# Optimization experiments

Hardware: AMD Instinct MI355X
Metric: run time of the kernel (lower is better)

## Reference

```python
import jax, jax.numpy as jnp
import numpy as np

EMBED_DIM = 128
HEADS = 4
HEAD_DIM = EMBED_DIM // HEADS
HIDDEN = EMBED_DIM * 4


def setup_inputs() -> dict:
    key = jax.random.key(0)
    ks = jax.random.split(key, 12)
    s = 0.02
    return {
        "x": jax.random.normal(ks[0], (4, 4096, EMBED_DIM), dtype=jnp.float32),
        "ln1_g": jnp.ones((EMBED_DIM,), jnp.float32),
        "ln1_b": jnp.zeros((EMBED_DIM,), jnp.float32),
        "qkv_w": jax.random.normal(ks[1], (EMBED_DIM, 3 * EMBED_DIM), jnp.float32) * s,
        "qkv_b": jnp.zeros((3 * EMBED_DIM,), jnp.float32),
        "proj_w": jax.random.normal(ks[2], (EMBED_DIM, EMBED_DIM), jnp.float32) * s,
        "proj_b": jnp.zeros((EMBED_DIM,), jnp.float32),
        "ln2_g": jnp.ones((EMBED_DIM,), jnp.float32),
        "ln2_b": jnp.zeros((EMBED_DIM,), jnp.float32),
        "mlp_w1": jax.random.normal(ks[3], (EMBED_DIM, HIDDEN), jnp.float32) * s,
        "mlp_b1": jnp.zeros((HIDDEN,), jnp.float32),
        "mlp_w2": jax.random.normal(ks[4], (HIDDEN, EMBED_DIM), jnp.float32) * s,
        "mlp_b2": jnp.zeros((EMBED_DIM,), jnp.float32),
    }


def _layernorm(x, g, b, eps=1e-5):
    mu = jnp.mean(x, axis=-1, keepdims=True)
    var = jnp.var(x, axis=-1, keepdims=True)
    return (x - mu) * jax.lax.rsqrt(var + eps) * g + b


def _msa(x, qkv_w, qkv_b, proj_w, proj_b):
    B, N, C = x.shape
    qkv = x @ qkv_w + qkv_b                       # [B,N,3C]
    qkv = qkv.reshape(B, N, 3, HEADS, HEAD_DIM)
    q, k, v = jnp.moveaxis(qkv, 2, 0)             # each [B,N,H,D]
    # scores: [B,H,N,N]
    attn = jnp.einsum("bnhd,bmhd->bhnm", q, k) / jnp.sqrt(jnp.float32(HEAD_DIM))
    attn = jax.nn.softmax(attn, axis=-1)
    out = jnp.einsum("bhnm,bmhd->bnhd", attn, v).reshape(B, N, C)
    return out @ proj_w + proj_b


def reference(x, ln1_g, ln1_b, qkv_w, qkv_b, proj_w, proj_b,
              ln2_g, ln2_b, mlp_w1, mlp_b1, mlp_w2, mlp_b2):
    # dropout is identity in eval mode
    x = x + _msa(_layernorm(x, ln1_g, ln1_b), qkv_w, qkv_b, proj_w, proj_b)
    h = _layernorm(x, ln2_g, ln2_b)
    h = jax.nn.gelu(h @ mlp_w1 + mlp_b1, approximate=False)
    x = x + (h @ mlp_w2 + mlp_b2)
    return x
```

## Files before the change

kernel.cpp:

```cpp
#include <hip/hip_runtime.h>
#include <hip/hip_bf16.h>
#include <math.h>

#define NSEQ   4096
#define CDIM   128
#define HD     32

typedef __attribute__((ext_vector_type(8))) short short8;
typedef __attribute__((ext_vector_type(4))) short short4v;
typedef __attribute__((ext_vector_type(4))) float f32x4;

#define QSCL (0.17677669529663687f * 1.4426950408889634f)

__device__ inline unsigned short f2bf(float f){
  union { float f; unsigned u; } v; v.f = f;
  return (unsigned short)((v.u + 0x7fffu + ((v.u >> 16) & 1u)) >> 16);
}
__device__ inline float bf2f(unsigned short u){
  union { unsigned u; float f; } v; v.u = ((unsigned)u) << 16;
  return v.f;
}
__device__ inline void gload_lds16(const unsigned short* g, unsigned short* l){
  __builtin_amdgcn_global_load_lds(
      (const __attribute__((address_space(1))) void*)g,
      (__attribute__((address_space(3))) void*)l, 16, 0, 0);
}


__global__ __launch_bounds__(256) void k_pack(
    const float* __restrict__ qkv_w, const float* __restrict__ qkv_b,
    const float* __restrict__ proj_w, const float* __restrict__ mlp_w1,
    const float* __restrict__ mlp_w2, unsigned short* __restrict__ wpack,
    float* __restrict__ bqs)
{
  const int gt = blockIdx.x * 256 + threadIdx.x;
  const int tile = gt >> 6, lane = gt & 63;
  const float* src; int N, KT, toff, dstoff; float scale = 1.f;
  if (tile < 96)       { src = qkv_w;  N = 384; KT = 4;  toff = tile;       dstoff = 0; }
  else if (tile < 128) { src = proj_w; N = 128; KT = 4;  toff = tile - 96;  dstoff = 49152; }
  else if (tile < 256) { src = mlp_w1; N = 512; KT = 4;  toff = tile - 128; dstoff = 65536; }
  else                 { src = mlp_w2; N = 128; KT = 16; toff = tile - 256; dstoff = 131072; }
  const int ct = toff / KT, kt = toff % KT;
  if (tile < 96 && ct < 8) scale = QSCL;
  const int row0 = kt * 32 + (lane >> 4) * 8, col = ct * 16 + (lane & 15);
  short8 v;
  #pragma unroll
  for (int i = 0; i < 8; i++)
    v[i] = (short)f2bf(src[(size_t)(row0 + i) * N + col] * scale);
  *(short8*)(wpack + dstoff + ((size_t)(ct * KT + kt) * 64 + lane) * 8) = v;
  if (gt < 384) bqs[gt] = qkv_b[gt] * (gt < 128 ? QSCL : 1.f);
}

__global__ __launch_bounds__(512) void k_qkv(
    const float* __restrict__ x, const float* __restrict__ g,
    const float* __restrict__ b, const unsigned short* __restrict__ wpack,
    const float* __restrict__ bqs, unsigned short* __restrict__ qkv)
{
  __shared__ unsigned short xn[64 * 128];
  const int tid = threadIdx.x;
  const int tok0 = blockIdx.x * 64;
  {
    const int grp = tid >> 5, l = tid & 31;
    #pragma unroll
    for (int it = 0; it < 4; it++){
      const int t = it * 16 + grp;
      const float4 xv = *(const float4*)(x + (size_t)(tok0 + t) * 128 + l * 4);
      float s  = xv.x + xv.y + xv.z + xv.w;
      float s2 = xv.x*xv.x + xv.y*xv.y + xv.z*xv.z + xv.w*xv.w;
      #pragma unroll
      for (int m = 1; m <= 16; m <<= 1){ s += __shfl_xor(s, m); s2 += __shfl_xor(s2, m); }
      const float mu = s * (1.f/128.f);
      const float rs = rsqrtf(s2 * (1.f/128.f) - mu*mu + 1e-5f);
      const int e = l * 4;
      const float4 gv = *(const float4*)(g + e), bv = *(const float4*)(b + e);
      short4v pk;
      pk[0] = (short)f2bf((xv.x - mu)*rs*gv.x + bv.x);
      pk[1] = (short)f2bf((xv.y - mu)*rs*gv.y + bv.y);
      pk[2] = (short)f2bf((xv.z - mu)*rs*gv.z + bv.z);
      pk[3] = (short)f2bf((xv.w - mu)*rs*gv.w + bv.w);
      const int bl = l >> 1;
      const int slot = bl * 64 + (t & 48) + ((t & 15) ^ bl);
      *(short4v*)(xn + slot * 8 + (l & 1) * 4) = pk;
    }
  }
  __syncthreads();
  const int wv = tid >> 6, lane = tid & 63, r = lane & 15, cg = lane >> 4;
  const int rt = wv & 3, ct0 = (wv >> 2) * 12;
  short8 af[4];
  #pragma unroll
  for (int kt = 0; kt < 4; kt++){
    const int bl = kt * 4 + cg;
    const int slot = bl * 64 + rt * 16 + (r ^ bl);
    af[kt] = *(const short8*)(xn + slot * 8);
  }
  const int bidx = tok0 >> 12, nloc = (tok0 & (NSEQ - 1)) + rt * 16 + cg * 4;
  for (int ct = ct0; ct < ct0 + 12; ct++){
    f32x4 acc = {0.f, 0.f, 0.f, 0.f};
    const unsigned short* bp = wpack + ((size_t)(ct * 4) * 64 + lane) * 8;
    #pragma unroll
    for (int kt = 0; kt < 4; kt++)
      acc = __builtin_amdgcn_mfma_f32_16x16x32_bf16(af[kt], *(const short8*)(bp + kt * 512), acc, 0, 0, 0);
    const int col = ct * 16 + r;
    const float bi = bqs[col];
    if (ct < 8){
      const int cc = col & 127, h = cc >> 5, d = cc & 31;
      unsigned short* plane = qkv + ((size_t)bidx * 4 + h) * (NSEQ * HD);
      #pragma unroll
      for (int reg = 0; reg < 4; reg++)
        plane[(size_t)(nloc + reg) * HD + d] = f2bf(acc[reg] + bi);
    } else if (ct < 16){
      const int cc = col & 127, h = cc >> 5, d = cc & 31;
      unsigned short* plane = qkv + ((size_t)16 + bidx * 4 + h) * (NSEQ * HD);
      const int t16 = ((tok0 & (NSEQ - 1)) >> 4) + rt;
      #pragma unroll
      for (int reg = 0; reg < 4; reg++)
        plane[(size_t)t16 * 512 + (d >> 3) * 128 + (cg * 4 + reg) * 8 + (d & 7)]
            = f2bf(acc[reg] + bi);
    } else {
      const int vct = ct - 16, h = vct >> 1, half = vct & 1;
      unsigned short* plane = qkv + ((size_t)32 + bidx * 4 + h) * (NSEQ * HD);
      const size_t ntile = (size_t)((tok0 & (NSEQ - 1)) >> 5) + (rt >> 1);
      const size_t vo = (ntile * 2 + half) * 512 + lane * 8 + (rt & 1) * 4;
      short4v pk;
      #pragma unroll
      for (int reg = 0; reg < 4; reg++) pk[reg] = (short)f2bf(acc[reg] + bi);
      *(short4v*)(plane + vo) = pk;
    }
  }
}

__global__ __launch_bounds__(512) void k_attn(
    const unsigned short* __restrict__ qkv, unsigned short* __restrict__ attnA)
{
  __shared__ unsigned short sbuf[16384];
  const int tid = threadIdx.x;
  const int lane = tid & 63, wv = tid >> 6;
  const int id = blockIdx.x;
  const int xcd = id & 7, seq = id >> 3;
  const int bh = xcd * 2 + (seq >> 4);
  const int qbase = (seq & 15) * 256 + wv * 32;
  const unsigned short* Q  = qkv + (size_t)bh * (NSEQ * HD);
  const unsigned short* Kc = qkv + (size_t)(16 + bh) * (NSEQ * HD);
  const unsigned short* Vc = qkv + (size_t)(32 + bh) * (NSEQ * HD);
  const int r = lane & 15, cg = lane >> 4;
  const short8 qf0 = *(const short8*)(Q + (size_t)(qbase + r) * HD + cg * 8);
  const short8 qf1 = *(const short8*)(Q + (size_t)(qbase + 16 + r) * HD + cg * 8);
  const unsigned short* gsrc = (wv < 4 ? Kc + wv * 512 : Vc + (wv - 4) * 512) + lane * 8;
  const int dst = wv * 512;
  union { unsigned u[4]; short8 s; } onesu;
  onesu.u[0] = 0x3F803F80u; onesu.u[1] = 0x3F803F80u;
  onesu.u[2] = 0x3F803F80u; onesu.u[3] = 0x3F803F80u;
  const short8 vones = onesu.s;
  f32x4 o00 = {0.f,0.f,0.f,0.f}, o01 = {0.f,0.f,0.f,0.f};
  f32x4 o10 = {0.f,0.f,0.f,0.f}, o11 = {0.f,0.f,0.f,0.f};
  f32x4 lacc0 = {0.f,0.f,0.f,0.f}, lacc1 = {0.f,0.f,0.f,0.f};
  const f32x4 zero = {0.f,0.f,0.f,0.f};
  gload_lds16(gsrc,        sbuf + 0 * 4096 + dst);
  gload_lds16(gsrc + 2048, sbuf + 1 * 4096 + dst);
  gload_lds16(gsrc + 4096, sbuf + 2 * 4096 + dst);
  for (int t = 0; t < 64; t++){
    asm volatile("s_waitcnt vmcnt(2) lgkmcnt(0)" ::: "memory");
    __builtin_amdgcn_sched_barrier(0);
    __builtin_amdgcn_s_barrier();
    __builtin_amdgcn_sched_barrier(0);
    const int tn = (t + 3 > 63) ? 63 : t + 3;
    gload_lds16(gsrc + (size_t)tn * 2048, sbuf + ((t + 3) & 3) * 4096 + dst);
    const unsigned short* skb = sbuf + (t & 3) * 4096;
    const unsigned short* svb = skb + 2048;
    #pragma unroll
    for (int ktp = 0; ktp < 2; ktp++){
      const short8 kaa = *(const short8*)(skb + (ktp * 2 + 0) * 512 + lane * 8);
      const short8 kab = *(const short8*)(skb + (ktp * 2 + 1) * 512 + lane * 8);
      const short8 va0 = *(const short8*)(svb + (ktp * 2 + 0) * 512 + lane * 8);
      const short8 va1 = *(const short8*)(svb + (ktp * 2 + 1) * 512 + lane * 8);
      const f32x4 s00 = __builtin_amdgcn_mfma_f32_16x16x32_bf16(kaa, qf0, zero, 0, 0, 0);
      const f32x4 s01 = __builtin_amdgcn_mfma_f32_16x16x32_bf16(kab, qf0, zero, 0, 0, 0);
      const f32x4 s10 = __builtin_amdgcn_mfma_f32_16x16x32_bf16(kaa, qf1, zero, 0, 0, 0);
      const f32x4 s11 = __builtin_amdgcn_mfma_f32_16x16x32_bf16(kab, qf1, zero, 0, 0, 0);
      float p00[4], p01[4], p10[4], p11[4];
      #pragma unroll
      for (int i = 0; i < 4; i++){
        p00[i] = __builtin_amdgcn_exp2f(s00[i]);
        p01[i] = __builtin_amdgcn_exp2f(s01[i]);
        p10[i] = __builtin_amdgcn_exp2f(s10[i]);
        p11[i] = __builtin_amdgcn_exp2f(s11[i]);
      }
      unsigned c0, c1, c2, c3, c4, c5, c6, c7;
      asm("v_cvt_pk_bf16_f32 %0, %1, %2" : "=v"(c0) : "v"(p00[0]), "v"(p00[1]));
      asm("v_cvt_pk_bf16_f32 %0, %1, %2" : "=v"(c1) : "v"(p00[2]), "v"(p00[3]));
      asm("v_cvt_pk_bf16_f32 %0, %1, %2" : "=v"(c2) : "v"(p01[0]), "v"(p01[1]));
      asm("v_cvt_pk_bf16_f32 %0, %1, %2" : "=v"(c3) : "v"(p01[2]), "v"(p01[3]));
      asm("v_cvt_pk_bf16_f32 %0, %1, %2" : "=v"(c4) : "v"(p10[0]), "v"(p10[1]));
      asm("v_cvt_pk_bf16_f32 %0, %1, %2" : "=v"(c5) : "v"(p10[2]), "v"(p10[3]));
      asm("v_cvt_pk_bf16_f32 %0, %1, %2" : "=v"(c6) : "v"(p11[0]), "v"(p11[1]));
      asm("v_cvt_pk_bf16_f32 %0, %1, %2" : "=v"(c7) : "v"(p11[2]), "v"(p11[3]));
      union { unsigned u[4]; short8 s; } pa, pb;
      pa.u[0] = c0; pa.u[1] = c1; pa.u[2] = c2; pa.u[3] = c3;
      pb.u[0] = c4; pb.u[1] = c5; pb.u[2] = c6; pb.u[3] = c7;
      o00 = __builtin_amdgcn_mfma_f32_16x16x32_bf16(va0, pa.s, o00, 0, 0, 0);
      o01 = __builtin_amdgcn_mfma_f32_16x16x32_bf16(va1, pa.s, o01, 0, 0, 0);
      o10 = __builtin_amdgcn_mfma_f32_16x16x32_bf16(va0, pb.s, o10, 0, 0, 0);
      o11 = __builtin_amdgcn_mfma_f32_16x16x32_bf16(va1, pb.s, o11, 0, 0, 0);
      lacc0 = __builtin_amdgcn_mfma_f32_16x16x32_bf16(vones, pa.s, lacc0, 0, 0, 0);
      lacc1 = __builtin_amdgcn_mfma_f32_16x16x32_bf16(vones, pb.s, lacc1, 0, 0, 0);
    }
  }
  asm volatile("s_waitcnt vmcnt(0)" ::: "memory");
  const float inv0 = 1.f / lacc0[0], inv1 = 1.f / lacc1[0];
  const int b = bh >> 2, h = bh & 3;
  unsigned short* pa = attnA + ((((size_t)b * NSEQ + qbase) >> 4) * 2048);
  short4v w0, w1, w2, w3;
  #pragma unroll
  for (int j = 0; j < 4; j++){
    w0[j] = (short)f2bf(o00[j] * inv0);
    w1[j] = (short)f2bf(o01[j] * inv0);
    w2[j] = (short)f2bf(o10[j] * inv1);
    w3[j] = (short)f2bf(o11[j] * inv1);
  }
  *(short4v*)(pa + (h * 4 + 0) * 128 + r * 8 + cg * 4)        = w0;
  *(short4v*)(pa + (h * 4 + 2) * 128 + r * 8 + cg * 4)        = w1;
  *(short4v*)(pa + 2048 + (h * 4 + 0) * 128 + r * 8 + cg * 4) = w2;
  *(short4v*)(pa + 2048 + (h * 4 + 2) * 128 + r * 8 + cg * 4) = w3;
}

__global__ __launch_bounds__(512, 6) void k_fused(
    const unsigned short* __restrict__ attnA, const float* __restrict__ x,
    const unsigned short* __restrict__ wpack, const float* __restrict__ pb,
    const float* __restrict__ g2, const float* __restrict__ b2,
    const float* __restrict__ b1, const float* __restrict__ b2m,
    float* __restrict__ out)
{
  __shared__ unsigned short afh[2][2048];
  __shared__ unsigned short sbb[32 * 128];
  __shared__ unsigned short afr[2][8192];
  const int tid = threadIdx.x, tok0 = blockIdx.x * 32;
  const int wv = tid >> 6, lane = tid & 63, r = lane & 15, cg = lane >> 4;
  const int rt = wv & 1, cgp = wv >> 1;
  {
    short8 af[4];
    const unsigned short* pa = attnA + ((size_t)((tok0 >> 4) + rt)) * 2048;
    #pragma unroll
    for (int kt = 0; kt < 4; kt++)
      af[kt] = *(const short8*)(pa + (kt * 4 + cg) * 128 + r * 8);
    const unsigned short* wp = wpack + 49152;
    for (int ct = cgp * 2; ct < cgp * 2 + 2; ct++){
      f32x4 acc = {0.f, 0.f, 0.f, 0.f};
      const unsigned short* bp = wp + ((size_t)(ct * 4) * 64 + lane) * 8;
      #pragma unroll
      for (int kt = 0; kt < 4; kt++)
        acc = __builtin_amdgcn_mfma_f32_16x16x32_bf16(af[kt], *(const short8*)(bp + kt * 512), acc, 0, 0, 0);
      const int col = ct * 16 + r;
      const float bi = pb[col];
      #pragma unroll
      for (int reg = 0; reg < 4; reg++){
        const int tl = rt * 16 + cg * 4 + reg;
        sbb[tl * 128 + col] = f2bf(acc[reg] + bi + x[(size_t)(tok0 + tl) * 128 + col]);
      }
    }
  }
  __syncthreads();
  {
    const int grp = tid >> 5, l = tid & 31;
    #pragma unroll
    for (int it = 0; it < 2; it++){
      const int t = it * 16 + grp;
      const short4v xb = *(const short4v*)(sbb + t * 128 + l * 4);
      const float x0 = bf2f((unsigned short)xb[0]), x1 = bf2f((unsigned short)xb[1]);
      const float x2 = bf2f((unsigned short)xb[2]), x3 = bf2f((unsigned short)xb[3]);
      float s  = x0 + x1 + x2 + x3;
      float s2 = x0*x0 + x1*x1 + x2*x2 + x3*x3;
      #pragma unroll
      for (int m = 1; m <= 16; m <<= 1){ s += __shfl_xor(s, m); s2 += __shfl_xor(s2, m); }
      const float mu = s * (1.f/128.f);
      const float rs = rsqrtf(s2 * (1.f/128.f) - mu*mu + 1e-5f);
      const int e = l * 4;
      const float4 gv = *(const float4*)(g2 + e), bv = *(const float4*)(b2 + e);
      short4v pk;
      pk[0] = (short)f2bf((x0 - mu)*rs*gv.x + bv.x);
      pk[1] = (short)f2bf((x1 - mu)*rs*gv.y + bv.y);
      pk[2] = (short)f2bf((x2 - mu)*rs*gv.z + bv.z);
      pk[3] = (short)f2bf((x3 - mu)*rs*gv.w + bv.w);
      *(short4v*)(&afh[t >> 4][(e >> 3) * 128 + (t & 15) * 8 + (e & 7)]) = pk;
    }
  }
  __syncthreads();
  {
    short8 hf[4];
    #pragma unroll
    for (int kt = 0; kt < 4; kt++)
      hf[kt] = *(const short8*)(&afh[rt][(kt * 4 + cg) * 128 + r * 8]);
    const unsigned short* w1 = wpack + 65536;
    for (int ct = cgp * 8; ct < cgp * 8 + 8; ct++){
      f32x4 acc = {0.f, 0.f, 0.f, 0.f};
      const unsigned short* bp = w1 + ((size_t)(ct * 4) * 64 + lane) * 8;
      #pragma unroll
      for (int kt = 0; kt < 4; kt++)
        acc = __builtin_amdgcn_mfma_f32_16x16x32_bf16(hf[kt], *(const short8*)(bp + kt * 512), acc, 0, 0, 0);
      const int col = ct * 16 + r;
      const float bi = b1[col];
      #pragma unroll
      for (int reg = 0; reg < 4; reg++){
        const float v = acc[reg] + bi;
        const float u = v * (2.3022077f + 0.10294324f * v * v);
        const float ge = v * __builtin_amdgcn_rcpf(1.f + __builtin_amdgcn_exp2f(-u));
        afr[rt][(col >> 3) * 128 + (cg * 4 + reg) * 8 + (col & 7)] = f2bf(ge);
      }
    }
  }
  __syncthreads();
  {
    const unsigned short* w2 = wpack + 131072;
    f32x4 acc0 = {0.f,0.f,0.f,0.f}, acc1 = {0.f,0.f,0.f,0.f};
    for (int kt = 0; kt < 16; kt++){
      const short8 a3 = *(const short8*)(&afr[rt][(kt * 4 + cg) * 128 + r * 8]);
      const unsigned short* bp0 = w2 + ((size_t)((cgp * 2 + 0) * 16 + kt) * 64 + lane) * 8;
      const unsigned short* bp1 = w2 + ((size_t)((cgp * 2 + 1) * 16 + kt) * 64 + lane) * 8;
      acc0 = __builtin_amdgcn_mfma_f32_16x16x32_bf16(a3, *(const short8*)(bp0), acc0, 0, 0, 0);
      acc1 = __builtin_amdgcn_mfma_f32_16x16x32_bf16(a3, *(const short8*)(bp1), acc1, 0, 0, 0);
    }
    #pragma unroll
    for (int c = 0; c < 2; c++){
      const f32x4 acc = c ? acc1 : acc0;
      const int col = (cgp * 2 + c) * 16 + r;
      const float bi = b2m[col];
      #pragma unroll
      for (int reg = 0; reg < 4; reg++){
        const int tl = rt * 16 + cg * 4 + reg;
        out[(size_t)(tok0 + tl) * 128 + col] = acc[reg] + bi + bf2f(sbb[tl * 128 + col]);
      }
    }
  }
}

extern "C" void kernel_launch(void* const* d_in, const int* in_sizes, int n_in,
                              void* d_out, int out_size, void* d_ws, size_t ws_size,
                              hipStream_t stream)
{
  const float* x      = (const float*)d_in[0];
  const float* ln1_g  = (const float*)d_in[1];
  const float* ln1_b  = (const float*)d_in[2];
  const float* qkv_w  = (const float*)d_in[3];
  const float* qkv_b  = (const float*)d_in[4];
  const float* proj_w = (const float*)d_in[5];
  const float* proj_b = (const float*)d_in[6];
  const float* ln2_g  = (const float*)d_in[7];
  const float* ln2_b  = (const float*)d_in[8];
  const float* mlp_w1 = (const float*)d_in[9];
  const float* mlp_b1 = (const float*)d_in[10];
  const float* mlp_w2 = (const float*)d_in[11];
  const float* mlp_b2 = (const float*)d_in[12];

  char* ws = (char*)d_ws;
  unsigned short* wpack = (unsigned short*)(ws);
  float*          bqs   = (float*)(ws + 393216);
  unsigned short* qkv   = (unsigned short*)(ws + 524288);
  unsigned short* attnA = (unsigned short*)(ws + 13107200);
  float* out = (float*)d_out;

  hipLaunchKernelGGL(k_pack, dim3(96), dim3(256), 0, stream,
                     qkv_w, qkv_b, proj_w, mlp_w1, mlp_w2, wpack, bqs);
  hipLaunchKernelGGL(k_qkv, dim3(256), dim3(512), 0, stream,
                     x, ln1_g, ln1_b, wpack, bqs, qkv);
  hipLaunchKernelGGL(k_attn, dim3(256), dim3(512), 0, stream, qkv, attnA);
  hipLaunchKernelGGL(k_fused, dim3(512), dim3(512), 0, stream,
                     attnA, x, wpack, proj_b, ln2_g, ln2_b,
                     mlp_b1, mlp_b2, out);
}
```

Baseline: 81.05 us.

## Retile attention to one query tile per wave and double grid size

The attention kernel now gives each wave 16 queries instead of 32. The grid doubles to 512 blocks. Each pipeline stage loads 256 keys and values into a 64KB LDS ring, using half the loop iterations. The aim is more blocks and waves per CU to hide latency and fill the device, at the cost of half the K/V reuse per wave, double total LDS read traffic, and a larger shared-memory footprint that may limit residency.

```diff
diff --git a/kernel.cpp b/kernel.cpp
--- a/kernel.cpp
+++ b/kernel.cpp
@@ -132,95 +132,81 @@
 __global__ __launch_bounds__(512) void k_attn(
     const unsigned short* __restrict__ qkv, unsigned short* __restrict__ attnA)
 {
-  __shared__ unsigned short sbuf[16384];
+  __shared__ unsigned short sbuf[32768];
   const int tid = threadIdx.x;
   const int lane = tid & 63, wv = tid >> 6;
   const int id = blockIdx.x;
   const int xcd = id & 7, seq = id >> 3;
-  const int bh = xcd * 2 + (seq >> 4);
-  const int qbase = (seq & 15) * 256 + wv * 32;
+  const int bh = xcd * 2 + (seq >> 5);
+  const int qbase = (seq & 31) * 128 + wv * 16;
   const unsigned short* Q  = qkv + (size_t)bh * (NSEQ * HD);
   const unsigned short* Kc = qkv + (size_t)(16 + bh) * (NSEQ * HD);
   const unsigned short* Vc = qkv + (size_t)(32 + bh) * (NSEQ * HD);
   const int r = lane & 15, cg = lane >> 4;
   const short8 qf0 = *(const short8*)(Q + (size_t)(qbase + r) * HD + cg * 8);
-  const short8 qf1 = *(const short8*)(Q + (size_t)(qbase + 16 + r) * HD + cg * 8);
-  const unsigned short* gsrc = (wv < 4 ? Kc + wv * 512 : Vc + (wv - 4) * 512) + lane * 8;
-  const int dst = wv * 512;
+  const unsigned short* gK = Kc + lane * 8;
+  const unsigned short* gV = Vc + lane * 8;
+  const int dK = wv * 512, dV = 4096 + wv * 512;
   union { unsigned u[4]; short8 s; } onesu;
   onesu.u[0] = 0x3F803F80u; onesu.u[1] = 0x3F803F80u;
   onesu.u[2] = 0x3F803F80u; onesu.u[3] = 0x3F803F80u;
   const short8 vones = onesu.s;
   f32x4 o00 = {0.f,0.f,0.f,0.f}, o01 = {0.f,0.f,0.f,0.f};
-  f32x4 o10 = {0.f,0.f,0.f,0.f}, o11 = {0.f,0.f,0.f,0.f};
-  f32x4 lacc0 = {0.f,0.f,0.f,0.f}, lacc1 = {0.f,0.f,0.f,0.f};
+  f32x4 lacc = {0.f,0.f,0.f,0.f};
   const f32x4 zero = {0.f,0.f,0.f,0.f};
-  gload_lds16(gsrc,        sbuf + 0 * 4096 + dst);
-  gload_lds16(gsrc + 2048, sbuf + 1 * 4096 + dst);
-  gload_lds16(gsrc + 4096, sbuf + 2 * 4096 + dst);
-  for (int t = 0; t < 64; t++){
-    asm volatile("s_waitcnt vmcnt(2) lgkmcnt(0)" ::: "memory");
+  #pragma unroll
+  for (int s = 0; s < 3; s++){
+    gload_lds16(gK + (size_t)(8 * s + wv) * 512, sbuf + s * 8192 + dK);
+    gload_lds16(gV + (size_t)(8 * s + wv) * 512, sbuf + s * 8192 + dV);
+  }
+  for (int t = 0; t < 32; t++){
+    asm volatile("s_waitcnt vmcnt(4) lgkmcnt(0)" ::: "memory");
     __builtin_amdgcn_sched_barrier(0);
     __builtin_amdgcn_s_barrier();
     __builtin_amdgcn_sched_barrier(0);
-    const int tn = (t + 3 > 63) ? 63 : t + 3;
-    gload_lds16(gsrc + (size_t)tn * 2048, sbuf + ((t + 3) & 3) * 4096 + dst);
-    const unsigned short* skb = sbuf + (t & 3) * 4096;
-    const unsigned short* svb = skb + 2048;
-    #pragma unroll
-    for (int ktp = 0; ktp < 2; ktp++){
+    const int tn = (t + 3 > 31) ? 31 : t + 3;
+    gload_lds16(gK + (size_t)(8 * tn + wv) * 512, sbuf + ((t + 3) & 3) * 8192 + dK);
+    gload_lds16(gV + (size_t)(8 * tn + wv) * 512, sbuf + ((t + 3) & 3) * 8192 + dV);
+    const unsigned short* skb = sbuf + (t & 3) * 8192;
+    const unsigned short* svb = skb + 4096;
+    #pragma unroll
+    for (int ktp = 0; ktp < 4; ktp++){
       const short8 kaa = *(const short8*)(skb + (ktp * 2 + 0) * 512 + lane * 8);
       const short8 kab = *(const short8*)(skb + (ktp * 2 + 1) * 512 + lane * 8);
-      const short8 va0 = *(const short8*)(svb + (ktp * 2 + 0) * 512 + lane * 8);
-      const short8 va1 = *(const short8*)(svb + (ktp * 2 + 1) * 512 + lane * 8);
+      const short8 va0 = *(const short8*)(svb + ktp * 1024 + lane * 8);
+      const short8 va1 = *(const short8*)(svb + ktp * 1024 + 512 + lane * 8);
       const f32x4 s00 = __builtin_amdgcn_mfma_f32_16x16x32_bf16(kaa, qf0, zero, 0, 0, 0);
       const f32x4 s01 = __builtin_amdgcn_mfma_f32_16x16x32_bf16(kab, qf0, zero, 0, 0, 0);
-      const f32x4 s10 = __builtin_amdgcn_mfma_f32_16x16x32_bf16(kaa, qf1, zero, 0, 0, 0);
-      const f32x4 s11 = __builtin_amdgcn_mfma_f32_16x16x32_bf16(kab, qf1, zero, 0, 0, 0);
-      float p00[4], p01[4], p10[4], p11[4];
+      float p0[4], p1[4];
       #pragma unroll
       for (int i = 0; i < 4; i++){
-        p00[i] = __builtin_amdgcn_exp2f(s00[i]);
-        p01[i] = __builtin_amdgcn_exp2f(s01[i]);
-        p10[i] = __builtin_amdgcn_exp2f(s10[i]);
-        p11[i] = __builtin_amdgcn_exp2f(s11[i]);
+        p0[i] = __builtin_amdgcn_exp2f(s00[i]);
+        p1[i] = __builtin_amdgcn_exp2f(s01[i]);
       }
-      unsigned c0, c1, c2, c3, c4, c5, c6, c7;
-      asm("v_cvt_pk_bf16_f32 %0, %1, %2" : "=v"(c0) : "v"(p00[0]), "v"(p00[1]));
-      asm("v_cvt_pk_bf16_f32 %0, %1, %2" : "=v"(c1) : "v"(p00[2]), "v"(p00[3]));
-      asm("v_cvt_pk_bf16_f32 %0, %1, %2" : "=v"(c2) : "v"(p01[0]), "v"(p01[1]));
-      asm("v_cvt_pk_bf16_f32 %0, %1, %2" : "=v"(c3) : "v"(p01[2]), "v"(p01[3]));
-      asm("v_cvt_pk_bf16_f32 %0, %1, %2" : "=v"(c4) : "v"(p10[0]), "v"(p10[1]));
-      asm("v_cvt_pk_bf16_f32 %0, %1, %2" : "=v"(c5) : "v"(p10[2]), "v"(p10[3]));
-      asm("v_cvt_pk_bf16_f32 %0, %1, %2" : "=v"(c6) : "v"(p11[0]), "v"(p11[1]));
-      asm("v_cvt_pk_bf16_f32 %0, %1, %2" : "=v"(c7) : "v"(p11[2]), "v"(p11[3]));
-      union { unsigned u[4]; short8 s; } pa, pb;
+      unsigned c0, c1, c2, c3;
+      asm("v_cvt_pk_bf16_f32 %0, %1, %2" : "=v"(c0) : "v"(p0[0]), "v"(p0[1]));
+      asm("v_cvt_pk_bf16_f32 %0, %1, %2" : "=v"(c1) : "v"(p0[2]), "v"(p0[3]));
+      asm("v_cvt_pk_bf16_f32 %0, %1, %2" : "=v"(c2) : "v"(p1[0]), "v"(p1[1]));
+      asm("v_cvt_pk_bf16_f32 %0, %1, %2" : "=v"(c3) : "v"(p1[2]), "v"(p1[3]));
+      union { unsigned u[4]; short8 s; } pa;
       pa.u[0] = c0; pa.u[1] = c1; pa.u[2] = c2; pa.u[3] = c3;
-      pb.u[0] = c4; pb.u[1] = c5; pb.u[2] = c6; pb.u[3] = c7;
       o00 = __builtin_amdgcn_mfma_f32_16x16x32_bf16(va0, pa.s, o00, 0, 0, 0);
       o01 = __builtin_amdgcn_mfma_f32_16x16x32_bf16(va1, pa.s, o01, 0, 0, 0);
-      o10 = __builtin_amdgcn_mfma_f32_16x16x32_bf16(va0, pb.s, o10, 0, 0, 0);
-      o11 = __builtin_amdgcn_mfma_f32_16x16x32_bf16(va1, pb.s, o11, 0, 0, 0);
-      lacc0 = __builtin_amdgcn_mfma_f32_16x16x32_bf16(vones, pa.s, lacc0, 0, 0, 0);
-      lacc1 = __builtin_amdgcn_mfma_f32_16x16x32_bf16(vones, pb.s, lacc1, 0, 0, 0);
+      lacc = __builtin_amdgcn_mfma_f32_16x16x32_bf16(vones, pa.s, lacc, 0, 0, 0);
     }
   }
   asm volatile("s_waitcnt vmcnt(0)" ::: "memory");
-  const float inv0 = 1.f / lacc0[0], inv1 = 1.f / lacc1[0];
+  const float inv = 1.f / lacc[0];
   const int b = bh >> 2, h = bh & 3;
   unsigned short* pa = attnA + ((((size_t)b * NSEQ + qbase) >> 4) * 2048);
-  short4v w0, w1, w2, w3;
+  short4v w0, w1;
   #pragma unroll
   for (int j = 0; j < 4; j++){
-    w0[j] = (short)f2bf(o00[j] * inv0);
-    w1[j] = (short)f2bf(o01[j] * inv0);
-    w2[j] = (short)f2bf(o10[j] * inv1);
-    w3[j] = (short)f2bf(o11[j] * inv1);
-  }
-  *(short4v*)(pa + (h * 4 + 0) * 128 + r * 8 + cg * 4)        = w0;
-  *(short4v*)(pa + (h * 4 + 2) * 128 + r * 8 + cg * 4)        = w1;
-  *(short4v*)(pa + 2048 + (h * 4 + 0) * 128 + r * 8 + cg * 4) = w2;
-  *(short4v*)(pa + 2048 + (h * 4 + 2) * 128 + r * 8 + cg * 4) = w3;
+    w0[j] = (short)f2bf(o00[j] * inv);
+    w1[j] = (short)f2bf(o01[j] * inv);
+  }
+  *(short4v*)(pa + (h * 4 + 0 + (cg >> 1)) * 128 + r * 8 + (cg & 1) * 4) = w0;
+  *(short4v*)(pa + (h * 4 + 2 + (cg >> 1)) * 128 + r * 8 + (cg & 1) * 4) = w1;
 }
 
 __global__ __launch_bounds__(512, 6) void k_fused(
@@ -361,7 +347,7 @@
                      qkv_w, qkv_b, proj_w, mlp_w1, mlp_w2, wpack, bqs);
   hipLaunchKernelGGL(k_qkv, dim3(256), dim3(512), 0, stream,
                      x, ln1_g, ln1_b, wpack, bqs, qkv);
-  hipLaunchKernelGGL(k_attn, dim3(256), dim3(512), 0, stream, qkv, attnA);
+  hipLaunchKernelGGL(k_attn, dim3(512), dim3(512), 0, stream, qkv, attnA);
   hipLaunchKernelGGL(k_fused, dim3(512), dim3(512), 0, stream,
                      attnA, x, wpack, proj_b, ln2_g, ln2_b,
                      mlp_b1, mlp_b2, out);
```

After: 84.06 us. 1.04x slower.
